# Optimization experiments

Hardware: AMD Instinct MI355X
Metric: run time of the kernel (lower is better)

## Reference

```python
import jax, jax.numpy as jnp
import numpy as np

N_QUBITS = 4
N_LAYERS = 3
DIM = 2 ** N_QUBITS  # 16
BATCH = 524288

# CNOT ring permutations: wire 0 is the MOST significant bit (PennyLane default.qubit).
# CNOT(c,t) maps basis index j -> j ^ (target_mask * control_bit(j)); it is its own inverse,
# so new_state[:, j] = old_state[:, perm[j]] with the same perm.
_idx = np.arange(DIM)

def _cnot_perm(c, t):
    cbit = (_idx >> (N_QUBITS - 1 - c)) & 1
    return _idx ^ (cbit << (N_QUBITS - 1 - t))

CNOT_PERMS = [jnp.asarray(_cnot_perm(i, (i + 1) % N_QUBITS)) for i in range(N_QUBITS)]

# PauliZ signs per wire: +1 if bit is 0, -1 if bit is 1. Shape (4, 16).
Z_SIGNS = jnp.asarray(
    np.stack([1.0 - 2.0 * ((_idx >> (N_QUBITS - 1 - w)) & 1) for w in range(N_QUBITS)]).astype(np.float32)
)


def _bcast(v):
    # angle-derived factor: scalar stays scalar, batched (B,) -> (B,1,1)
    return v[:, None, None] if jnp.ndim(v) else v


def _apply_ry(state, wire, theta):
    # state: (B, 16) complex64; theta: scalar or (B,)
    B = state.shape[0]
    half = theta * 0.5
    c, s = _bcast(jnp.cos(half)), _bcast(jnp.sin(half))
    st = state.reshape(B, 2 ** wire, 2, 2 ** (N_QUBITS - 1 - wire))
    a0, a1 = st[:, :, 0, :], st[:, :, 1, :]
    return jnp.stack([c * a0 - s * a1, s * a0 + c * a1], axis=2).reshape(B, DIM)


def _apply_rz(state, wire, theta):
    # RZ = diag(e^{-i t/2}, e^{+i t/2})
    B = state.shape[0]
    half = theta * 0.5
    ch, sh = jnp.cos(half), jnp.sin(half)
    p0, p1 = _bcast(ch - 1j * sh), _bcast(ch + 1j * sh)
    st = state.reshape(B, 2 ** wire, 2, 2 ** (N_QUBITS - 1 - wire))
    return jnp.stack([p0 * st[:, :, 0, :], p1 * st[:, :, 1, :]], axis=2).reshape(B, DIM)


def setup_inputs() -> dict:
    key = jax.random.key(0)
    kx, kw = jax.random.split(key)
    x = jax.random.normal(kx, (BATCH, N_QUBITS), dtype=jnp.float32)
    weights = jax.random.normal(kw, (N_LAYERS, N_QUBITS, 2), dtype=jnp.float32) * 0.1
    return {"x": x, "weights": weights}


def reference(x, weights):
    B = x.shape[0]
    state = jnp.zeros((B, DIM), dtype=jnp.complex64).at[:, 0].set(1.0)
    # input-encoding RY rotations (batched angles)
    for i in range(N_QUBITS):
        state = _apply_ry(state, i, x[:, i])
    for layer in range(N_LAYERS):
        for i in range(N_QUBITS):
            state = state[:, CNOT_PERMS[i]]
        for i in range(N_QUBITS):
            state = _apply_ry(state, i, weights[layer, i, 0])
            state = _apply_rz(state, i, weights[layer, i, 1])
    probs = jnp.real(state) ** 2 + jnp.imag(state) ** 2  # (B, 16) float32
    return probs @ Z_SIGNS.T  # (B, 4) <Z_w> expectation values
```

## Files before the change

kernel.cpp:

```cpp
#include <hip/hip_runtime.h>
#include <math.h>

#define DIM 16
#define NQ 4
#define NL 3
#define VQC_BATCH 524288

__global__ __launch_bounds__(64) void vqc_prep(const float* __restrict__ w,
                                               float* __restrict__ U) {
  const int col = threadIdx.x;
  if (col >= DIM) return;
  float sr[DIM], si[DIM];
#pragma unroll
  for (int k = 0; k < DIM; ++k) { sr[k] = (k == col) ? 1.f : 0.f; si[k] = 0.f; }

#pragma unroll
  for (int layer = 0; layer < NL; ++layer) {
#pragma unroll
    for (int c = 0; c < NQ; ++c) {
      const int t = (c + 1) & 3;
      float tr[DIM], ti[DIM];
#pragma unroll
      for (int idx = 0; idx < DIM; ++idx) {
        const int cbit = (idx >> (3 - c)) & 1;
        const int src = idx ^ (cbit << (3 - t));
        tr[idx] = sr[src]; ti[idx] = si[src];
      }
#pragma unroll
      for (int idx = 0; idx < DIM; ++idx) { sr[idx] = tr[idx]; si[idx] = ti[idx]; }
    }
#pragma unroll
    for (int q = 0; q < NQ; ++q) {
      const int m = 8 >> q;
      {
        float s, c;
        __sincosf(0.5f * w[(layer * NQ + q) * 2 + 0], &s, &c);
#pragma unroll
        for (int idx = 0; idx < DIM; ++idx) {
          if ((idx & m) == 0) {
            const int i1 = idx | m;
            const float a0r = sr[idx], a0i = si[idx];
            const float a1r = sr[i1], a1i = si[i1];
            sr[idx] = c * a0r - s * a1r;  si[idx] = c * a0i - s * a1i;
            sr[i1]  = s * a0r + c * a1r;  si[i1]  = s * a0i + c * a1i;
          }
        }
      }
      {
        float sh, ch;
        __sincosf(0.5f * w[(layer * NQ + q) * 2 + 1], &sh, &ch);
#pragma unroll
        for (int idx = 0; idx < DIM; ++idx) {
          const float ar = sr[idx], ai = si[idx];
          if (idx & m) { sr[idx] = ch * ar - sh * ai; si[idx] = ch * ai + sh * ar; }
          else         { sr[idx] = ch * ar + sh * ai; si[idx] = ch * ai - sh * ar; }
        }
      }
    }
  }
#pragma unroll
  for (int j = 0; j < DIM; ++j) {
    U[(j * DIM + col) * 2 + 0] = sr[j];
    U[(j * DIM + col) * 2 + 1] = si[j];
  }
}

__global__ __launch_bounds__(256) void vqc_main(const float4* __restrict__ x4,
                                                const float4* __restrict__ U4,
                                                float4* __restrict__ out4) {
  const int b = blockIdx.x * 256 + threadIdx.x;
  const float4 xv = x4[b];

  float s0, c0, s1, c1, s2, c2, s3, c3;
  __sincosf(0.5f * xv.x, &s0, &c0);
  __sincosf(0.5f * xv.y, &s1, &c1);
  __sincosf(0.5f * xv.z, &s2, &c2);
  __sincosf(0.5f * xv.w, &s3, &c3);

  float ab[4], cd[4];
  ab[0] = c0 * c1; ab[1] = c0 * s1; ab[2] = s0 * c1; ab[3] = s0 * s1;
  cd[0] = c2 * c3; cd[1] = c2 * s3; cd[2] = s2 * c3; cd[3] = s2 * s3;
  float sv[DIM];
#pragma unroll
  for (int hi = 0; hi < 4; ++hi)
#pragma unroll
    for (int lo = 0; lo < 4; ++lo)
      sv[hi * 4 + lo] = ab[hi] * cd[lo];

  float p[DIM];
#pragma unroll
  for (int j = 0; j < DIM; ++j) {
    float vr = 0.f, vi = 0.f;
#pragma unroll
    for (int iv = 0; iv < 8; ++iv) {
      const float4 u = U4[j * 8 + iv];
      vr = __builtin_fmaf(u.x, sv[2 * iv], vr);
      vi = __builtin_fmaf(u.y, sv[2 * iv], vi);
      vr = __builtin_fmaf(u.z, sv[2 * iv + 1], vr);
      vi = __builtin_fmaf(u.w, sv[2 * iv + 1], vi);
    }
    p[j] = vr * vr + vi * vi;
  }

  float a[8], z3 = 0.f;
#pragma unroll
  for (int t = 0; t < 8; ++t) { a[t] = p[2 * t] + p[2 * t + 1]; z3 += p[2 * t] - p[2 * t + 1]; }
  float b2[4], z2 = 0.f;
#pragma unroll
  for (int t = 0; t < 4; ++t) { b2[t] = a[2 * t] + a[2 * t + 1]; z2 += a[2 * t] - a[2 * t + 1]; }
  const float e0 = b2[0] + b2[1], e1 = b2[2] + b2[3];
  const float z1 = (b2[0] - b2[1]) + (b2[2] - b2[3]);
  const float z0 = e0 - e1;

  out4[b] = make_float4(z0, z1, z2, z3);
}

extern "C" void kernel_launch(void* const* d_in, const int* in_sizes, int n_in,
                              void* d_out, int out_size, void* d_ws, size_t ws_size,
                              hipStream_t stream) {
  const float* x = (const float*)d_in[0];
  const float* w = (const float*)d_in[1];
  float* U = (float*)d_ws;

  vqc_prep<<<1, 64, 0, stream>>>(w, U);
  vqc_main<<<VQC_BATCH / 256, 256, 0, stream>>>((const float4*)x, (const float4*)U,
                                                (float4*)d_out);
}
```

Before: 72.39 us.

## Fuse unitary build into main kernel with LDS and two elements per thread

Removes the separate single-block prep kernel. Each block of the fused kernel now rebuilds the 16x16 unitary in shared memory from the weights, then syncs before using it. Each thread handles two batch elements so every shared-memory read of U feeds twice as many FMAs. The cost is that every block redoes the unitary construction with only 16 active threads ahead of a barrier, and register pressure rises.

```diff
diff --git a/kernel.cpp b/kernel.cpp
--- a/kernel.cpp
+++ b/kernel.cpp
@@ -1,19 +1,18 @@
 #include <hip/hip_runtime.h>
-#include <math.h>
 
 #define DIM 16
 #define NQ 4
 #define NL 3
 #define VQC_BATCH 524288
+#define TPB 256
+#define EPT 2
+#define EPB (TPB * EPT)
 
-__global__ __launch_bounds__(64) void vqc_prep(const float* __restrict__ w,
-                                               float* __restrict__ U) {
-  const int col = threadIdx.x;
-  if (col >= DIM) return;
-  float sr[DIM], si[DIM];
+__device__ __forceinline__ void build_U_column(const float* __restrict__ w,
+                                               int col, float sr[DIM],
+                                               float si[DIM]) {
 #pragma unroll
   for (int k = 0; k < DIM; ++k) { sr[k] = (k == col) ? 1.f : 0.f; si[k] = 0.f; }
-
 #pragma unroll
   for (int layer = 0; layer < NL; ++layer) {
 #pragma unroll
@@ -33,8 +32,8 @@
     for (int q = 0; q < NQ; ++q) {
       const int m = 8 >> q;
       {
-        float s, c;
-        __sincosf(0.5f * w[(layer * NQ + q) * 2 + 0], &s, &c);
+        const float th = 0.5f * w[(layer * NQ + q) * 2 + 0];
+        const float s = __sinf(th), c = __cosf(th);
 #pragma unroll
         for (int idx = 0; idx < DIM; ++idx) {
           if ((idx & m) == 0) {
@@ -47,8 +46,8 @@
         }
       }
       {
-        float sh, ch;
-        __sincosf(0.5f * w[(layer * NQ + q) * 2 + 1], &sh, &ch);
+        const float ph = 0.5f * w[(layer * NQ + q) * 2 + 1];
+        const float sh = __sinf(ph), ch = __cosf(ph);
 #pragma unroll
         for (int idx = 0; idx < DIM; ++idx) {
           const float ar = sr[idx], ai = si[idx];
@@ -58,50 +57,24 @@
       }
     }
   }
-#pragma unroll
-  for (int j = 0; j < DIM; ++j) {
-    U[(j * DIM + col) * 2 + 0] = sr[j];
-    U[(j * DIM + col) * 2 + 1] = si[j];
-  }
 }
 
-__global__ __launch_bounds__(256) void vqc_main(const float4* __restrict__ x4,
-                                                const float4* __restrict__ U4,
-                                                float4* __restrict__ out4) {
-  const int b = blockIdx.x * 256 + threadIdx.x;
-  const float4 xv = x4[b];
-
-  float s0, c0, s1, c1, s2, c2, s3, c3;
-  __sincosf(0.5f * xv.x, &s0, &c0);
-  __sincosf(0.5f * xv.y, &s1, &c1);
-  __sincosf(0.5f * xv.z, &s2, &c2);
-  __sincosf(0.5f * xv.w, &s3, &c3);
-
+__device__ __forceinline__ void state_from_x(const float4 xv, float sv[DIM]) {
+  const float s0 = __sinf(0.5f * xv.x), c0 = __cosf(0.5f * xv.x);
+  const float s1 = __sinf(0.5f * xv.y), c1 = __cosf(0.5f * xv.y);
+  const float s2 = __sinf(0.5f * xv.z), c2 = __cosf(0.5f * xv.z);
+  const float s3 = __sinf(0.5f * xv.w), c3 = __cosf(0.5f * xv.w);
   float ab[4], cd[4];
   ab[0] = c0 * c1; ab[1] = c0 * s1; ab[2] = s0 * c1; ab[3] = s0 * s1;
   cd[0] = c2 * c3; cd[1] = c2 * s3; cd[2] = s2 * c3; cd[3] = s2 * s3;
-  float sv[DIM];
 #pragma unroll
   for (int hi = 0; hi < 4; ++hi)
 #pragma unroll
     for (int lo = 0; lo < 4; ++lo)
       sv[hi * 4 + lo] = ab[hi] * cd[lo];
+}
 
-  float p[DIM];
-#pragma unroll
-  for (int j = 0; j < DIM; ++j) {
-    float vr = 0.f, vi = 0.f;
-#pragma unroll
-    for (int iv = 0; iv < 8; ++iv) {
-      const float4 u = U4[j * 8 + iv];
-      vr = __builtin_fmaf(u.x, sv[2 * iv], vr);
-      vi = __builtin_fmaf(u.y, sv[2 * iv], vi);
-      vr = __builtin_fmaf(u.z, sv[2 * iv + 1], vr);
-      vi = __builtin_fmaf(u.w, sv[2 * iv + 1], vi);
-    }
-    p[j] = vr * vr + vi * vi;
-  }
-
+__device__ __forceinline__ float4 z_from_p(const float p[DIM]) {
   float a[8], z3 = 0.f;
 #pragma unroll
   for (int t = 0; t < 8; ++t) { a[t] = p[2 * t] + p[2 * t + 1]; z3 += p[2 * t] - p[2 * t + 1]; }
@@ -111,8 +84,54 @@
   const float e0 = b2[0] + b2[1], e1 = b2[2] + b2[3];
   const float z1 = (b2[0] - b2[1]) + (b2[2] - b2[3]);
   const float z0 = e0 - e1;
+  return make_float4(z0, z1, z2, z3);
+}
 
-  out4[b] = make_float4(z0, z1, z2, z3);
+__global__ __launch_bounds__(TPB) void vqc_fused(const float4* __restrict__ x4,
+                                                 const float* __restrict__ w,
+                                                 float4* __restrict__ out4) {
+  __shared__ float Uld[DIM * DIM * 2];
+
+  const int tid = threadIdx.x;
+  if (tid < DIM) {
+    float sr[DIM], si[DIM];
+    build_U_column(w, tid, sr, si);
+#pragma unroll
+    for (int j = 0; j < DIM; ++j) {
+      Uld[(j * DIM + tid) * 2 + 0] = sr[j];
+      Uld[(j * DIM + tid) * 2 + 1] = si[j];
+    }
+  }
+  __syncthreads();
+  const float4* U4 = (const float4*)Uld;
+
+  const int e0 = blockIdx.x * EPB + tid;
+  const int e1 = e0 + TPB;
+
+  float sv0[DIM], sv1[DIM];
+  state_from_x(x4[e0], sv0);
+  state_from_x(x4[e1], sv1);
+
+  float p0[DIM], p1[DIM];
+#pragma unroll
+  for (int j = 0; j < DIM; ++j) {
+    float vr0 = 0.f, vi0 = 0.f, vr1 = 0.f, vi1 = 0.f;
+#pragma unroll
+    for (int iv = 0; iv < 8; ++iv) {
+      const float4 u = U4[j * 8 + iv];
+      const float a0 = sv0[2 * iv], b0 = sv0[2 * iv + 1];
+      const float a1 = sv1[2 * iv], b1 = sv1[2 * iv + 1];
+      vr0 = __builtin_fmaf(u.x, a0, vr0); vi0 = __builtin_fmaf(u.y, a0, vi0);
+      vr0 = __builtin_fmaf(u.z, b0, vr0); vi0 = __builtin_fmaf(u.w, b0, vi0);
+      vr1 = __builtin_fmaf(u.x, a1, vr1); vi1 = __builtin_fmaf(u.y, a1, vi1);
+      vr1 = __builtin_fmaf(u.z, b1, vr1); vi1 = __builtin_fmaf(u.w, b1, vi1);
+    }
+    p0[j] = vr0 * vr0 + vi0 * vi0;
+    p1[j] = vr1 * vr1 + vi1 * vi1;
+  }
+
+  out4[e0] = z_from_p(p0);
+  out4[e1] = z_from_p(p1);
 }
 
 extern "C" void kernel_launch(void* const* d_in, const int* in_sizes, int n_in,
@@ -120,9 +139,6 @@
                               hipStream_t stream) {
   const float* x = (const float*)d_in[0];
   const float* w = (const float*)d_in[1];
-  float* U = (float*)d_ws;
-
-  vqc_prep<<<1, 64, 0, stream>>>(w, U);
-  vqc_main<<<VQC_BATCH / 256, 256, 0, stream>>>((const float4*)x, (const float4*)U,
-                                                (float4*)d_out);
+  vqc_fused<<<VQC_BATCH / EPB, TPB, 0, stream>>>((const float4*)x, w,
+                                                 (float4*)d_out);
 }
```

Result: slower. 91.90 us (+27.0%).
